# Kernel optimization log

Measured on AMD Instinct MI355X. Metric: run time of the kernel, lower is better.

The kernel has to match this reference:

```python
import jax, jax.numpy as jnp
import numpy as np

N_NODES = 100000
N_RAND_EDGES = 6400000
N_EDGES = N_RAND_EDGES + N_NODES  # + self loops (dgl.add_self_loop)
IN_FEATS, HIDDEN, N_CLASSES = 16, 8, 2


def setup_inputs() -> dict:
    key = jax.random.key(0)
    ks = jax.random.split(key, 8)
    x = jax.random.normal(ks[0], (N_NODES, IN_FEATS), dtype=jnp.float32)
    src_r = jax.random.randint(ks[1], (N_RAND_EDGES,), 0, N_NODES, dtype=jnp.int32)
    dst_r = jax.random.randint(ks[2], (N_RAND_EDGES,), 0, N_NODES, dtype=jnp.int32)
    loop = jnp.arange(N_NODES, dtype=jnp.int32)
    src = jnp.concatenate([src_r, loop])
    dst = jnp.concatenate([dst_r, loop])
    timestamp = jax.random.uniform(ks[3], (N_EDGES,), dtype=jnp.float32)
    W1 = jax.random.normal(ks[4], (IN_FEATS, HIDDEN), dtype=jnp.float32) / np.sqrt(IN_FEATS)
    b1 = jnp.zeros((HIDDEN,), dtype=jnp.float32)
    W2 = jax.random.normal(ks[5], (HIDDEN, N_CLASSES), dtype=jnp.float32) / np.sqrt(HIDDEN)
    b2 = jnp.zeros((N_CLASSES,), dtype=jnp.float32)
    return {"x": x, "src": src, "dst": dst, "timestamp": timestamp,
            "W1": W1, "b1": b1, "W2": W2, "b2": b2}


def _gcn_layer(h, src, dst, ts, W, b):
    # message: u_mul_e -> src feature scaled by scalar edge weight  [E, F]
    msg = h[src] * ts[:, None]
    # reduce: max over incoming edges per destination node
    agg = jax.ops.segment_max(msg, dst, num_segments=N_NODES)
    # DGL fills nodes with no in-edges with 0 (self-loops make this rare)
    agg = jnp.where(jnp.isfinite(agg), agg, 0.0)
    return agg @ W + b


def reference(x, src, dst, timestamp, W1, b1, W2, b2):
    h = _gcn_layer(x, src, dst, timestamp, W1, b1)
    h = jax.nn.relu(h)
    # dropout(p=0.5, train=False) -> identity in eval mode
    out = _gcn_layer(h, src, dst, timestamp, W2, b2)
    return out
```

## Files before the change

### kernel.cpp

```cpp
#include <hip/hip_runtime.h>
#include <hip/hip_bf16.h>

#define N_NODES 100000
#define N_EDGES 6500000
#define IN_FEATS 16
#define HIDDEN 8
#define N_CLASSES 2
#define BK 196
#define NBK 512
#define EPB 8192

__device__ __forceinline__ unsigned f2key(float f) {
    int i = __float_as_int(f);
    return (unsigned)(i ^ ((i >> 31) | 0x80000000));
}
__device__ __forceinline__ float key2f(unsigned u) {
    int i = (u & 0x80000000u) ? (int)(u ^ 0x80000000u) : (int)(~u);
    return __int_as_float(i);
}

__global__ void convert_x(const float* __restrict__ x, unsigned* __restrict__ xb) {
    int total = N_NODES * IN_FEATS / 2;
    for (int i = blockIdx.x * blockDim.x + threadIdx.x; i < total; i += gridDim.x * blockDim.x) {
        unsigned u0 = __float_as_uint(x[2 * i]);
        unsigned u1 = __float_as_uint(x[2 * i + 1]);
        unsigned r0 = (u0 + 0x7FFFu + ((u0 >> 16) & 1u)) >> 16;
        unsigned r1 = (u1 + 0x7FFFu + ((u1 >> 16) & 1u)) >> 16;
        xb[i] = r0 | (r1 << 16);
    }
}

__global__ __launch_bounds__(1024) void count_buckets(const int* __restrict__ dst,
                                                      unsigned* __restrict__ cnt) {
    __shared__ unsigned lcnt[NBK];
    int t = threadIdx.x;
    if (t < NBK) lcnt[t] = 0u;
    __syncthreads();
    int base = blockIdx.x * EPB;
#pragma unroll
    for (int k = 0; k < 8; ++k) {
        int e = base + k * 1024 + t;
        if (e < N_EDGES) {
            unsigned d = (unsigned)__builtin_nontemporal_load(&dst[e]);
            atomicAdd(&lcnt[d / BK], 1u);
        }
    }
    __syncthreads();
    if (t < NBK && lcnt[t]) atomicAdd(&cnt[t], lcnt[t]);
}

__global__ __launch_bounds__(NBK) void scan_starts(const unsigned* __restrict__ cnt,
                                                   unsigned* __restrict__ start,
                                                   unsigned* __restrict__ cursor) {
    __shared__ unsigned s[NBK];
    int t = threadIdx.x;
    unsigned c = cnt[t];
    s[t] = c;
    for (int d = 1; d < NBK; d <<= 1) {
        __syncthreads();
        unsigned add = (t >= d) ? s[t - d] : 0u;
        __syncthreads();
        s[t] += add;
    }
    unsigned excl = s[t] - c;
    start[t] = excl;
    cursor[t] = excl;
    if (t == NBK - 1) start[NBK] = excl + c;
}

__global__ __launch_bounds__(1024) void binfill(
    const int* __restrict__ src, const int* __restrict__ dst,
    const float* __restrict__ ts, unsigned* __restrict__ gcursor,
    uint2* __restrict__ binned) {
    __shared__ uint2 stage[EPB];
    __shared__ unsigned lcnt[NBK];
    __shared__ unsigned lstart[NBK + 1];
    __shared__ unsigned shift[NBK];
    unsigned* s = (unsigned*)stage;
    int t = threadIdx.x;
    if (t < NBK) lcnt[t] = 0u;
    __syncthreads();
    int base = blockIdx.x * EPB;
    unsigned bd[8], sv[8], tv[8], slot[8];
#pragma unroll
    for (int k = 0; k < 8; ++k) {
        int e = base + k * 1024 + t;
        if (e < N_EDGES) {
            unsigned d = (unsigned)__builtin_nontemporal_load(&dst[e]);
            unsigned b = d / BK;
            bd[k] = (b << 8) | (d - b * BK);
            sv[k] = (unsigned)__builtin_nontemporal_load(&src[e]);
            tv[k] = __float_as_uint(__builtin_nontemporal_load(&ts[e]));
            slot[k] = atomicAdd(&lcnt[b], 1u);
        }
    }
    __syncthreads();
    unsigned c = (t < NBK) ? lcnt[t] : 0u;
    s[t] = c;
#pragma unroll
    for (int d = 1; d < 1024; d <<= 1) {
        __syncthreads();
        unsigned add = (t >= d) ? s[t - d] : 0u;
        __syncthreads();
        s[t] += add;
    }
    __syncthreads();
    unsigned excl = s[t] - c;
    if (t < NBK) {
        lstart[t] = excl;
        unsigned gb = atomicAdd(&gcursor[t], c);
        shift[t] = gb - excl;
        if (t == NBK - 1) lstart[NBK] = excl + c;
    }
    __syncthreads();
#pragma unroll
    for (int k = 0; k < 8; ++k) {
        int e = base + k * 1024 + t;
        if (e < N_EDGES) {
            unsigned b = bd[k] >> 8;
            unsigned pos = lstart[b] + slot[k];
            stage[pos] = make_uint2(sv[k] | ((bd[k] & 255u) << 17), tv[k]);
        }
    }
    __syncthreads();
    unsigned total = lstart[NBK];
#pragma unroll
    for (int j = 0; j < 8; ++j) {
        unsigned i = (unsigned)t + j * 1024u;
        if (i < total) {
            unsigned lo = 0, hi = NBK - 1;
            while (lo < hi) {
                unsigned mid = (lo + hi + 1) >> 1;
                if (lstart[mid] <= i) lo = mid; else hi = mid - 1;
            }
            uint2 v = stage[i];
            __builtin_nontemporal_store(((unsigned long long)v.y << 32) | v.x,
                                        (unsigned long long*)&binned[i + shift[lo]]);
        }
    }
}

__global__ __launch_bounds__(1024) void layer1(
    const unsigned* __restrict__ start, const uint2* __restrict__ binned,
    const uint4* __restrict__ xb, const float* __restrict__ W1,
    const float* __restrict__ b1, float* __restrict__ h) {
    __shared__ unsigned tile[BK * 17];
    __shared__ float sW[IN_FEATS * HIDDEN];
    __shared__ float sb[HIDDEN];
    int t = threadIdx.x;
    if (t < IN_FEATS * HIDDEN) sW[t] = W1[t];
    if (t < HIDDEN) sb[t] = b1[t];
    for (int i = t; i < BK * 17; i += 1024) tile[i] = 0u;
    __syncthreads();
    unsigned e0 = start[blockIdx.x], e1 = start[blockIdx.x + 1];
    for (unsigned e = e0 + t; e < e1; e += 1024) {
        unsigned long long r = __builtin_nontemporal_load((const unsigned long long*)&binned[e]);
        unsigned rx = (unsigned)r;
        unsigned srow = rx & 0x1FFFFu;
        unsigned drow = rx >> 17;
        float tv = __uint_as_float((unsigned)(r >> 32));
        uint4 a = xb[srow * 2], b = xb[srow * 2 + 1];
        unsigned* row = tile + drow * 17;
#pragma unroll
        for (int w = 0; w < 8; ++w) {
            unsigned u = (w < 4) ? ((const unsigned*)&a)[w] : ((const unsigned*)&b)[w - 4];
            float f0 = __uint_as_float(u << 16) * tv;
            float f1 = __uint_as_float(u & 0xFFFF0000u) * tv;
            atomicMax(row + 2 * w,     f2key(f0));
            atomicMax(row + 2 * w + 1, f2key(f1));
        }
    }
    __syncthreads();
    int node = blockIdx.x * BK + t;
    if (t < BK && node < N_NODES) {
        float a[IN_FEATS];
#pragma unroll
        for (int f = 0; f < IN_FEATS; ++f) a[f] = key2f(tile[t * 17 + f]);
        float o[HIDDEN];
#pragma unroll
        for (int j = 0; j < HIDDEN; ++j) {
            float sacc = sb[j];
#pragma unroll
            for (int f = 0; f < IN_FEATS; ++f) sacc += a[f] * sW[f * HIDDEN + j];
            o[j] = fmaxf(sacc, 0.f);
        }
        float4* hp = (float4*)(h + (size_t)node * HIDDEN);
        hp[0] = make_float4(o[0], o[1], o[2], o[3]);
        hp[1] = make_float4(o[4], o[5], o[6], o[7]);
    }
}

__global__ __launch_bounds__(1024) void layer2(
    const unsigned* __restrict__ start, const uint2* __restrict__ binned,
    const float* __restrict__ h, const float* __restrict__ W2,
    const float* __restrict__ b2, float* __restrict__ out) {
    __shared__ unsigned tile[BK * 9];
    __shared__ float sW[HIDDEN * N_CLASSES];
    __shared__ float sb[N_CLASSES];
    int t = threadIdx.x;
    if (t < HIDDEN * N_CLASSES) sW[t] = W2[t];
    if (t < N_CLASSES) sb[t] = b2[t];
    for (int i = t; i < BK * 9; i += 1024) tile[i] = 0u;
    __syncthreads();
    unsigned e0 = start[blockIdx.x], e1 = start[blockIdx.x + 1];
    for (unsigned e = e0 + t; e < e1; e += 1024) {
        unsigned long long r = __builtin_nontemporal_load((const unsigned long long*)&binned[e]);
        unsigned rx = (unsigned)r;
        unsigned srow = rx & 0x1FFFFu;
        unsigned drow = rx >> 17;
        float tv = __uint_as_float((unsigned)(r >> 32));
        const float4* hs = (const float4*)(h + (size_t)srow * HIDDEN);
        float4 v0 = hs[0], v1 = hs[1];
        unsigned* row = tile + drow * 9;
        atomicMax(row + 0, f2key(v0.x * tv));
        atomicMax(row + 1, f2key(v0.y * tv));
        atomicMax(row + 2, f2key(v0.z * tv));
        atomicMax(row + 3, f2key(v0.w * tv));
        atomicMax(row + 4, f2key(v1.x * tv));
        atomicMax(row + 5, f2key(v1.y * tv));
        atomicMax(row + 6, f2key(v1.z * tv));
        atomicMax(row + 7, f2key(v1.w * tv));
    }
    __syncthreads();
    int node = blockIdx.x * BK + t;
    if (t < BK && node < N_NODES) {
        float a[HIDDEN];
#pragma unroll
        for (int f = 0; f < HIDDEN; ++f) a[f] = key2f(tile[t * 9 + f]);
        float o0 = sb[0], o1 = sb[1];
#pragma unroll
        for (int f = 0; f < HIDDEN; ++f) {
            o0 += a[f] * sW[f * N_CLASSES + 0];
            o1 += a[f] * sW[f * N_CLASSES + 1];
        }
        ((float2*)out)[node] = make_float2(o0, o1);
    }
}

__global__ void fb_init_keys(unsigned* __restrict__ k1, unsigned* __restrict__ k2) {
    int i = blockIdx.x * blockDim.x + threadIdx.x;
    for (int idx = i; idx < N_NODES * IN_FEATS; idx += gridDim.x * blockDim.x) k1[idx] = 0u;
    for (int idx = i; idx < N_NODES * HIDDEN; idx += gridDim.x * blockDim.x) k2[idx] = 0u;
}
__global__ void fb_scatter1(const int* __restrict__ src, const int* __restrict__ dst,
                            const float* __restrict__ ts, const float* __restrict__ x,
                            unsigned* __restrict__ agg) {
    int e = blockIdx.x * blockDim.x + threadIdx.x;
    if (e >= N_EDGES) return;
    int s = src[e]; int d = dst[e]; float t = ts[e];
    const float4* xs = (const float4*)(x + (size_t)s * IN_FEATS);
    unsigned* a = agg + (size_t)d * IN_FEATS;
#pragma unroll
    for (int q = 0; q < 4; ++q) {
        float4 v = xs[q];
        atomicMax(a + q * 4 + 0, f2key(v.x * t));
        atomicMax(a + q * 4 + 1, f2key(v.y * t));
        atomicMax(a + q * 4 + 2, f2key(v.z * t));
        atomicMax(a + q * 4 + 3, f2key(v.w * t));
    }
}
__global__ void fb_node1(const unsigned* __restrict__ agg, const float* __restrict__ W1,
                         const float* __restrict__ b1, float* __restrict__ h) {
    int n = blockIdx.x * blockDim.x + threadIdx.x;
    if (n >= N_NODES) return;
    float a[IN_FEATS];
#pragma unroll
    for (int f = 0; f < IN_FEATS; ++f) a[f] = key2f(agg[(size_t)n * IN_FEATS + f]);
#pragma unroll
    for (int j = 0; j < HIDDEN; ++j) {
        float acc = b1[j];
#pragma unroll
        for (int f = 0; f < IN_FEATS; ++f) acc += a[f] * W1[f * HIDDEN + j];
        h[(size_t)n * HIDDEN + j] = acc > 0.f ? acc : 0.f;
    }
}
__global__ void fb_scatter2(const int* __restrict__ src, const int* __restrict__ dst,
                            const float* __restrict__ ts, const float* __restrict__ h,
                            unsigned* __restrict__ agg) {
    int e = blockIdx.x * blockDim.x + threadIdx.x;
    if (e >= N_EDGES) return;
    int s = src[e]; int d = dst[e]; float t = ts[e];
    const float4* hs = (const float4*)(h + (size_t)s * HIDDEN);
    unsigned* a = agg + (size_t)d * HIDDEN;
#pragma unroll
    for (int q = 0; q < 2; ++q) {
        float4 v = hs[q];
        atomicMax(a + q * 4 + 0, f2key(v.x * t));
        atomicMax(a + q * 4 + 1, f2key(v.y * t));
        atomicMax(a + q * 4 + 2, f2key(v.z * t));
        atomicMax(a + q * 4 + 3, f2key(v.w * t));
    }
}
__global__ void fb_node2(const unsigned* __restrict__ agg, const float* __restrict__ W2,
                         const float* __restrict__ b2, float* __restrict__ out) {
    int n = blockIdx.x * blockDim.x + threadIdx.x;
    if (n >= N_NODES) return;
    float a[HIDDEN];
#pragma unroll
    for (int f = 0; f < HIDDEN; ++f) a[f] = key2f(agg[(size_t)n * HIDDEN + f]);
#pragma unroll
    for (int j = 0; j < N_CLASSES; ++j) {
        float acc = b2[j];
#pragma unroll
        for (int f = 0; f < HIDDEN; ++f) acc += a[f] * W2[f * N_CLASSES + j];
        out[(size_t)n * N_CLASSES + j] = acc;
    }
}

extern "C" void kernel_launch(void* const* d_in, const int* in_sizes, int n_in,
                              void* d_out, int out_size, void* d_ws, size_t ws_size,
                              hipStream_t stream) {
    const float* x  = (const float*)d_in[0];
    const int* src  = (const int*)d_in[1];
    const int* dst  = (const int*)d_in[2];
    const float* ts = (const float*)d_in[3];
    const float* W1 = (const float*)d_in[4];
    const float* b1 = (const float*)d_in[5];
    const float* W2 = (const float*)d_in[6];
    const float* b2 = (const float*)d_in[7];
    float* out = (float*)d_out;

    char* ws = (char*)d_ws;
    size_t off = 0;
    auto alloc = [&](size_t bytes) { char* p = ws + off; off += (bytes + 255) & ~(size_t)255; return p; };

    unsigned* cnt    = (unsigned*)alloc(NBK * 4);
    unsigned* start  = (unsigned*)alloc((NBK + 1) * 4);
    unsigned* cursor = (unsigned*)alloc(NBK * 4);
    uint2*    binned = (uint2*)alloc((size_t)N_EDGES * 8);
    float*    h      = (float*)alloc((size_t)N_NODES * HIDDEN * 4);
    unsigned* xb     = (unsigned*)alloc((size_t)N_NODES * IN_FEATS * 2);
    size_t fast_need = off;

    int eblocks = (N_EDGES + EPB - 1) / EPB;

    if (fast_need <= ws_size) {
        hipMemsetAsync(cnt, 0, NBK * 4, stream);
        convert_x<<<512, 256, 0, stream>>>(x, xb);
        count_buckets<<<eblocks, 1024, 0, stream>>>(dst, cnt);
        scan_starts<<<1, NBK, 0, stream>>>(cnt, start, cursor);
        binfill<<<eblocks, 1024, 0, stream>>>(src, dst, ts, cursor, binned);
        layer1<<<NBK, 1024, 0, stream>>>(start, binned, (const uint4*)xb, W1, b1, h);
        layer2<<<NBK, 1024, 0, stream>>>(start, binned, h, W2, b2, out);
    } else {
        unsigned* k1 = (unsigned*)d_ws;
        float* hh    = (float*)(k1 + (size_t)N_NODES * IN_FEATS);
        unsigned* k2 = (unsigned*)(hh + (size_t)N_NODES * HIDDEN);
        int eb = (N_EDGES + 255) / 256;
        fb_init_keys<<<2048, 256, 0, stream>>>(k1, k2);
        fb_scatter1<<<eb, 256, 0, stream>>>(src, dst, ts, x, k1);
        fb_node1<<<(N_NODES + 255) / 256, 256, 0, stream>>>(k1, W1, b1, hh);
        fb_scatter2<<<eb, 256, 0, stream>>>(src, dst, ts, hh, k2);
        fb_node2<<<(N_NODES + 255) / 256, 256, 0, stream>>>(k2, W2, b2, out);
    }
}
```

Measured before the change: 206.6 us.

## Store hidden layer in bf16, wave-scan binfill, unroll edge loops, add occupancy hints

The hidden activations are stored as packed bf16 (16 bytes per node instead of 32), which halves the gather traffic in layer2. binfill now packs bucket, row and slot into one register and defers the src/ts loads until after the scan, lowering register pressure. Its 1024-wide block scan is replaced by a wave-level shuffle scan. The edge loops in layer1 and layer2 process two edges per iteration so more loads are in flight, and launch_bounds gain a minimum-blocks hint. Rounding h to bf16 adds precision loss to the second layer.

Result: faster. 200.6 us (-2.9%).

```diff
diff --git a/kernel.cpp b/kernel.cpp
--- a/kernel.cpp
+++ b/kernel.cpp
@@ -18,20 +18,21 @@
     int i = (u & 0x80000000u) ? (int)(u ^ 0x80000000u) : (int)(~u);
     return __int_as_float(i);
 }
+__device__ __forceinline__ unsigned pack_bf16(float f0, float f1) {
+    unsigned u0 = __float_as_uint(f0), u1 = __float_as_uint(f1);
+    u0 = (u0 + 0x7FFFu + ((u0 >> 16) & 1u)) >> 16;
+    u1 = (u1 + 0x7FFFu + ((u1 >> 16) & 1u)) >> 16;
+    return u0 | (u1 << 16);
+}
 
 __global__ void convert_x(const float* __restrict__ x, unsigned* __restrict__ xb) {
     int total = N_NODES * IN_FEATS / 2;
-    for (int i = blockIdx.x * blockDim.x + threadIdx.x; i < total; i += gridDim.x * blockDim.x) {
-        unsigned u0 = __float_as_uint(x[2 * i]);
-        unsigned u1 = __float_as_uint(x[2 * i + 1]);
-        unsigned r0 = (u0 + 0x7FFFu + ((u0 >> 16) & 1u)) >> 16;
-        unsigned r1 = (u1 + 0x7FFFu + ((u1 >> 16) & 1u)) >> 16;
-        xb[i] = r0 | (r1 << 16);
-    }
-}
-
-__global__ __launch_bounds__(1024) void count_buckets(const int* __restrict__ dst,
-                                                      unsigned* __restrict__ cnt) {
+    for (int i = blockIdx.x * blockDim.x + threadIdx.x; i < total; i += gridDim.x * blockDim.x)
+        xb[i] = pack_bf16(x[2 * i], x[2 * i + 1]);
+}
+
+__global__ __launch_bounds__(1024, 8) void count_buckets(const int* __restrict__ dst,
+                                                         unsigned* __restrict__ cnt) {
     __shared__ unsigned lcnt[NBK];
     int t = threadIdx.x;
     if (t < NBK) lcnt[t] = 0u;
@@ -40,10 +41,7 @@
 #pragma unroll
     for (int k = 0; k < 8; ++k) {
         int e = base + k * 1024 + t;
-        if (e < N_EDGES) {
-            unsigned d = (unsigned)__builtin_nontemporal_load(&dst[e]);
-            atomicAdd(&lcnt[d / BK], 1u);
-        }
+        if (e < N_EDGES) atomicAdd(&lcnt[((unsigned)dst[e]) / BK], 1u);
     }
     __syncthreads();
     if (t < NBK && lcnt[t]) atomicAdd(&cnt[t], lcnt[t]);
@@ -68,58 +66,65 @@
     if (t == NBK - 1) start[NBK] = excl + c;
 }
 
-__global__ __launch_bounds__(1024) void binfill(
+__global__ __launch_bounds__(1024, 8) void binfill(
     const int* __restrict__ src, const int* __restrict__ dst,
     const float* __restrict__ ts, unsigned* __restrict__ gcursor,
     uint2* __restrict__ binned) {
     __shared__ uint2 stage[EPB];
     __shared__ unsigned lcnt[NBK];
     __shared__ unsigned lstart[NBK + 1];
-    __shared__ unsigned shift[NBK];
-    unsigned* s = (unsigned*)stage;
+    __shared__ unsigned shiftv[NBK];
+    __shared__ unsigned waveTot[8], waveBase[8];
     int t = threadIdx.x;
     if (t < NBK) lcnt[t] = 0u;
     __syncthreads();
     int base = blockIdx.x * EPB;
-    unsigned bd[8], sv[8], tv[8], slot[8];
+    unsigned pk[8];
 #pragma unroll
     for (int k = 0; k < 8; ++k) {
         int e = base + k * 1024 + t;
+        pk[k] = 0xFFFFFFFFu;
         if (e < N_EDGES) {
-            unsigned d = (unsigned)__builtin_nontemporal_load(&dst[e]);
+            unsigned d = (unsigned)dst[e];
             unsigned b = d / BK;
-            bd[k] = (b << 8) | (d - b * BK);
-            sv[k] = (unsigned)__builtin_nontemporal_load(&src[e]);
-            tv[k] = __float_as_uint(__builtin_nontemporal_load(&ts[e]));
-            slot[k] = atomicAdd(&lcnt[b], 1u);
+            unsigned slot = atomicAdd(&lcnt[b], 1u);
+            pk[k] = ((d - b * BK) << 22) | (b << 13) | slot;
         }
     }
     __syncthreads();
     unsigned c = (t < NBK) ? lcnt[t] : 0u;
-    s[t] = c;
-#pragma unroll
-    for (int d = 1; d < 1024; d <<= 1) {
-        __syncthreads();
-        unsigned add = (t >= d) ? s[t - d] : 0u;
-        __syncthreads();
-        s[t] += add;
-    }
-    __syncthreads();
-    unsigned excl = s[t] - c;
+    unsigned inc = c;
+    int lane = t & 63;
+#pragma unroll
+    for (int d = 1; d < 64; d <<= 1) {
+        unsigned v = __shfl_up(inc, d, 64);
+        if (lane >= d) inc += v;
+    }
+    if (t < NBK && lane == 63) waveTot[t >> 6] = inc;
+    __syncthreads();
+    if (t == 0) {
+        unsigned acc = 0;
+#pragma unroll
+        for (int w = 0; w < 8; ++w) { waveBase[w] = acc; acc += waveTot[w]; }
+    }
+    __syncthreads();
     if (t < NBK) {
+        unsigned excl = waveBase[t >> 6] + inc - c;
         lstart[t] = excl;
         unsigned gb = atomicAdd(&gcursor[t], c);
-        shift[t] = gb - excl;
+        shiftv[t] = gb - excl;
         if (t == NBK - 1) lstart[NBK] = excl + c;
     }
     __syncthreads();
 #pragma unroll
     for (int k = 0; k < 8; ++k) {
-        int e = base + k * 1024 + t;
-        if (e < N_EDGES) {
-            unsigned b = bd[k] >> 8;
-            unsigned pos = lstart[b] + slot[k];
-            stage[pos] = make_uint2(sv[k] | ((bd[k] & 255u) << 17), tv[k]);
+        if (pk[k] != 0xFFFFFFFFu) {
+            int e = base + k * 1024 + t;
+            unsigned b = (pk[k] >> 13) & 511u;
+            unsigned pos = lstart[b] + (pk[k] & 8191u);
+            unsigned sv = (unsigned)__builtin_nontemporal_load(&src[e]);
+            float tv = __builtin_nontemporal_load(&ts[e]);
+            stage[pos] = make_uint2(sv | ((pk[k] >> 22) << 17), __float_as_uint(tv));
         }
     }
     __syncthreads();
@@ -135,15 +140,26 @@
             }
             uint2 v = stage[i];
             __builtin_nontemporal_store(((unsigned long long)v.y << 32) | v.x,
-                                        (unsigned long long*)&binned[i + shift[lo]]);
-        }
-    }
-}
-
-__global__ __launch_bounds__(1024) void layer1(
+                                        (unsigned long long*)&binned[i + shiftv[lo]]);
+        }
+    }
+}
+
+__device__ __forceinline__ void agg16(unsigned* row, uint4 a, uint4 b, float tv) {
+    const unsigned* pa = (const unsigned*)&a;
+    const unsigned* pb = (const unsigned*)&b;
+#pragma unroll
+    for (int w = 0; w < 8; ++w) {
+        unsigned u = (w < 4) ? pa[w] : pb[w - 4];
+        atomicMax(row + 2 * w,     f2key(__uint_as_float(u << 16) * tv));
+        atomicMax(row + 2 * w + 1, f2key(__uint_as_float(u & 0xFFFF0000u) * tv));
+    }
+}
+
+__global__ __launch_bounds__(1024, 8) void layer1(
     const unsigned* __restrict__ start, const uint2* __restrict__ binned,
     const uint4* __restrict__ xb, const float* __restrict__ W1,
-    const float* __restrict__ b1, float* __restrict__ h) {
+    const float* __restrict__ b1, uint4* __restrict__ hb) {
     __shared__ unsigned tile[BK * 17];
     __shared__ float sW[IN_FEATS * HIDDEN];
     __shared__ float sb[HIDDEN];
@@ -153,22 +169,25 @@
     for (int i = t; i < BK * 17; i += 1024) tile[i] = 0u;
     __syncthreads();
     unsigned e0 = start[blockIdx.x], e1 = start[blockIdx.x + 1];
-    for (unsigned e = e0 + t; e < e1; e += 1024) {
-        unsigned long long r = __builtin_nontemporal_load((const unsigned long long*)&binned[e]);
-        unsigned rx = (unsigned)r;
-        unsigned srow = rx & 0x1FFFFu;
-        unsigned drow = rx >> 17;
-        float tv = __uint_as_float((unsigned)(r >> 32));
-        uint4 a = xb[srow * 2], b = xb[srow * 2 + 1];
-        unsigned* row = tile + drow * 17;
-#pragma unroll
-        for (int w = 0; w < 8; ++w) {
-            unsigned u = (w < 4) ? ((const unsigned*)&a)[w] : ((const unsigned*)&b)[w - 4];
-            float f0 = __uint_as_float(u << 16) * tv;
-            float f1 = __uint_as_float(u & 0xFFFF0000u) * tv;
-            atomicMax(row + 2 * w,     f2key(f0));
-            atomicMax(row + 2 * w + 1, f2key(f1));
-        }
+    unsigned e = e0 + t;
+    for (; e + 1024 < e1; e += 2048) {
+        unsigned long long r0 = __builtin_nontemporal_load((const unsigned long long*)&binned[e]);
+        unsigned long long r1 = __builtin_nontemporal_load((const unsigned long long*)&binned[e + 1024]);
+        unsigned s0 = (unsigned)r0 & 0x1FFFFu, d0 = ((unsigned)r0) >> 17;
+        unsigned s1 = (unsigned)r1 & 0x1FFFFu, d1 = ((unsigned)r1) >> 17;
+        float t0 = __uint_as_float((unsigned)(r0 >> 32));
+        float t1 = __uint_as_float((unsigned)(r1 >> 32));
+        uint4 a0 = xb[s0 * 2], c0 = xb[s0 * 2 + 1];
+        uint4 a1 = xb[s1 * 2], c1 = xb[s1 * 2 + 1];
+        agg16(tile + d0 * 17, a0, c0, t0);
+        agg16(tile + d1 * 17, a1, c1, t1);
+    }
+    if (e < e1) {
+        unsigned long long r0 = __builtin_nontemporal_load((const unsigned long long*)&binned[e]);
+        unsigned s0 = (unsigned)r0 & 0x1FFFFu, d0 = ((unsigned)r0) >> 17;
+        float t0 = __uint_as_float((unsigned)(r0 >> 32));
+        uint4 a0 = xb[s0 * 2], c0 = xb[s0 * 2 + 1];
+        agg16(tile + d0 * 17, a0, c0, t0);
     }
     __syncthreads();
     int node = blockIdx.x * BK + t;
@@ -184,15 +203,24 @@
             for (int f = 0; f < IN_FEATS; ++f) sacc += a[f] * sW[f * HIDDEN + j];
             o[j] = fmaxf(sacc, 0.f);
         }
-        float4* hp = (float4*)(h + (size_t)node * HIDDEN);
-        hp[0] = make_float4(o[0], o[1], o[2], o[3]);
-        hp[1] = make_float4(o[4], o[5], o[6], o[7]);
-    }
-}
-
-__global__ __launch_bounds__(1024) void layer2(
+        hb[node] = make_uint4(pack_bf16(o[0], o[1]), pack_bf16(o[2], o[3]),
+                              pack_bf16(o[4], o[5]), pack_bf16(o[6], o[7]));
+    }
+}
+
+__device__ __forceinline__ void agg8(unsigned* row, uint4 a, float tv) {
+    const unsigned* pa = (const unsigned*)&a;
+#pragma unroll
+    for (int w = 0; w < 4; ++w) {
+        unsigned u = pa[w];
+        atomicMax(row + 2 * w,     f2key(__uint_as_float(u << 16) * tv));
+        atomicMax(row + 2 * w + 1, f2key(__uint_as_float(u & 0xFFFF0000u) * tv));
+    }
+}
+
+__global__ __launch_bounds__(1024, 8) void layer2(
     const unsigned* __restrict__ start, const uint2* __restrict__ binned,
-    const float* __restrict__ h, const float* __restrict__ W2,
+    const uint4* __restrict__ hb, const float* __restrict__ W2,
     const float* __restrict__ b2, float* __restrict__ out) {
     __shared__ unsigned tile[BK * 9];
     __shared__ float sW[HIDDEN * N_CLASSES];
@@ -203,23 +231,24 @@
     for (int i = t; i < BK * 9; i += 1024) tile[i] = 0u;
     __syncthreads();
     unsigned e0 = start[blockIdx.x], e1 = start[blockIdx.x + 1];
-    for (unsigned e = e0 + t; e < e1; e += 1024) {
-        unsigned long long r = __builtin_nontemporal_load((const unsigned long long*)&binned[e]);
-        unsigned rx = (unsigned)r;
-        unsigned srow = rx & 0x1FFFFu;
-        unsigned drow = rx >> 17;
-        float tv = __uint_as_float((unsigned)(r >> 32));
-        const float4* hs = (const float4*)(h + (size_t)srow * HIDDEN);
-        float4 v0 = hs[0], v1 = hs[1];
-        unsigned* row = tile + drow * 9;
-        atomicMax(row + 0, f2key(v0.x * tv));
-        atomicMax(row + 1, f2key(v0.y * tv));
-        atomicMax(row + 2, f2key(v0.z * tv));
-        atomicMax(row + 3, f2key(v0.w * tv));
-        atomicMax(row + 4, f2key(v1.x * tv));
-        atomicMax(row + 5, f2key(v1.y * tv));
-        atomicMax(row + 6, f2key(v1.z * tv));
-        atomicMax(row + 7, f2key(v1.w * tv));
+    unsigned e = e0 + t;
+    for (; e + 1024 < e1; e += 2048) {
+        unsigned long long r0 = __builtin_nontemporal_load((const unsigned long long*)&binned[e]);
+        unsigned long long r1 = __builtin_nontemporal_load((const unsigned long long*)&binned[e + 1024]);
+        unsigned s0 = (unsigned)r0 & 0x1FFFFu, d0 = ((unsigned)r0) >> 17;
+        unsigned s1 = (unsigned)r1 & 0x1FFFFu, d1 = ((unsigned)r1) >> 17;
+        float t0 = __uint_as_float((unsigned)(r0 >> 32));
+        float t1 = __uint_as_float((unsigned)(r1 >> 32));
+        uint4 h0 = hb[s0];
+        uint4 h1 = hb[s1];
+        agg8(tile + d0 * 9, h0, t0);
+        agg8(tile + d1 * 9, h1, t1);
+    }
+    if (e < e1) {
+        unsigned long long r0 = __builtin_nontemporal_load((const unsigned long long*)&binned[e]);
+        unsigned s0 = (unsigned)r0 & 0x1FFFFu, d0 = ((unsigned)r0) >> 17;
+        float t0 = __uint_as_float((unsigned)(r0 >> 32));
+        agg8(tile + d0 * 9, hb[s0], t0);
     }
     __syncthreads();
     int node = blockIdx.x * BK + t;
@@ -328,7 +357,7 @@
     unsigned* start  = (unsigned*)alloc((NBK + 1) * 4);
     unsigned* cursor = (unsigned*)alloc(NBK * 4);
     uint2*    binned = (uint2*)alloc((size_t)N_EDGES * 8);
-    float*    h      = (float*)alloc((size_t)N_NODES * HIDDEN * 4);
+    uint4*    hb     = (uint4*)alloc((size_t)N_NODES * 16);
     unsigned* xb     = (unsigned*)alloc((size_t)N_NODES * IN_FEATS * 2);
     size_t fast_need = off;
 
@@ -340,8 +369,8 @@
         count_buckets<<<eblocks, 1024, 0, stream>>>(dst, cnt);
         scan_starts<<<1, NBK, 0, stream>>>(cnt, start, cursor);
         binfill<<<eblocks, 1024, 0, stream>>>(src, dst, ts, cursor, binned);
-        layer1<<<NBK, 1024, 0, stream>>>(start, binned, (const uint4*)xb, W1, b1, h);
-        layer2<<<NBK, 1024, 0, stream>>>(start, binned, h, W2, b2, out);
+        layer1<<<NBK, 1024, 0, stream>>>(start, binned, (const uint4*)xb, W1, b1, hb);
+        layer2<<<NBK, 1024, 0, stream>>>(start, binned, hb, W2, b2, out);
     } else {
         unsigned* k1 = (unsigned*)d_ws;
         float* hh    = (float*)(k1 + (size_t)N_NODES * IN_FEATS);
```
